# Kernel optimization log

Measured on AMD Instinct MI355X. Metric: run time of the kernel, lower is better.

The kernel has to match this reference:

```python
import jax, jax.numpy as jnp
import numpy as np

B, T, E = 4, 2048, 768
H = 12
D = E // H  # head dim = 64


def setup_inputs() -> dict:
    key = jax.random.key(0)
    ks = jax.random.split(key, 9)
    s = 0.02
    x = jax.random.normal(ks[0], (B, T, E), dtype=jnp.float32)
    Wq = jax.random.normal(ks[1], (E, E), dtype=jnp.float32) * s
    bq = jnp.zeros((E,), dtype=jnp.float32)
    Wk = jax.random.normal(ks[2], (E, E), dtype=jnp.float32) * s
    bk = jnp.zeros((E,), dtype=jnp.float32)
    Wv = jax.random.normal(ks[3], (E, E), dtype=jnp.float32) * s
    bv = jnp.zeros((E,), dtype=jnp.float32)
    Wo = jax.random.normal(ks[4], (E, E), dtype=jnp.float32) * s
    bo = jnp.zeros((E,), dtype=jnp.float32)
    # causal mask, broadcastable [1,1,T,T]; masked_fill where mask == 0
    attn_mask = jnp.tril(jnp.ones((T, T), dtype=jnp.int32))[None, None, :, :]
    return {"x": x, "Wq": Wq, "bq": bq, "Wk": Wk, "bk": bk,
            "Wv": Wv, "bv": bv, "Wo": Wo, "bo": bo, "attn_mask": attn_mask}


def reference(x, Wq, bq, Wk, bk, Wv, bv, Wo, bo, attn_mask):
    # QKV projections: [B,T,E] -> [B,T,E]
    q = x @ Wq + bq
    k = x @ Wk + bk
    v = x @ Wv + bv
    # split heads -> [B,H,T,D]
    def split(t):
        return t.reshape(B, T, H, D).transpose(0, 2, 1, 3)
    q, k, v = split(q), split(k), split(v)
    # eager attention: full [B,H,T,T] scores (faithful to the torch module)
    att = jnp.einsum('bhqd,bhkd->bhqk', q, k) * (1.0 / np.sqrt(D).astype(np.float32))
    att = jnp.where(attn_mask == 0, jnp.float32(-jnp.inf), att)
    att_weights = jax.nn.softmax(att, axis=-1)
    # attn_dropout rate = 0.0 (eval) -> identity
    y = jnp.einsum('bhqk,bhkd->bhqd', att_weights, v)
    y = y.transpose(0, 2, 1, 3).reshape(B, T, E)
    y = y @ Wo + bo  # proj_dropout rate = 0.0 -> identity
    return (y, att_weights)
```

## Files before the change

### kernel.cpp

```cpp
#include <hip/hip_runtime.h>
#include <hip/hip_bf16.h>
#include <stdint.h>

#define BB 4
#define HH 12
#define TT 2048
#define DD 64
#define EE 768
#define BT (BB*TT)
#define NQKV (3*EE)

typedef __attribute__((ext_vector_type(8))) short bf16x8;
typedef __attribute__((ext_vector_type(4))) float f32x4;

__device__ __forceinline__ unsigned short f2bf(float f){
  union { float f; unsigned int u; } x; x.f = f;
  unsigned int u = x.u;
  unsigned int r = (u + 0x7fffu + ((u >> 16) & 1u)) >> 16;
  return (unsigned short)r;
}

__global__ void cvt_bf16(const float* __restrict__ src, unsigned short* __restrict__ dst, int n){
  int i = (blockIdx.x*blockDim.x + threadIdx.x)*4;
  if (i < n){
    float4 v = *(const float4*)&src[i];
    ushort4 o;
    o.x = f2bf(v.x); o.y = f2bf(v.y); o.z = f2bf(v.z); o.w = f2bf(v.w);
    *(ushort4*)&dst[i] = o;
  }
}

__global__ void transpose_cvt_768(const float* __restrict__ src,
                                  unsigned short* __restrict__ dst){
  __shared__ float tile[32][33];
  int bx = blockIdx.x*32, by = blockIdx.y*32;
  int tx = threadIdx.x, ty = threadIdx.y;
  #pragma unroll
  for (int i=0;i<32;i+=8) tile[ty+i][tx] = src[(size_t)(by+ty+i)*EE + bx+tx];
  __syncthreads();
  #pragma unroll
  for (int i=0;i<32;i+=8) dst[(size_t)(bx+ty+i)*EE + by+tx] = f2bf(tile[tx][ty+i]);
}

__device__ __forceinline__ void gemm_core_128(
    const unsigned short* __restrict__ A, const unsigned short* __restrict__ Bt,
    int K, int mBase, int nBase,
    unsigned short* Alds, unsigned short* Blds,
    f32x4 acc[4][4])
{
  const int tid = threadIdx.x;
  const int lane = tid & 63, wave = tid >> 6;
  const int wm = wave & 1, wn = wave >> 1;
  const int ln15 = lane & 15, quad = lane >> 4;
  #pragma unroll
  for (int mt=0; mt<4; ++mt)
    #pragma unroll
    for (int nt=0; nt<4; ++nt)
      acc[mt][nt] = (f32x4){0.f,0.f,0.f,0.f};

  for (int k0=0; k0<K; k0+=32){
    #pragma unroll
    for (int i=0;i<2;i++){
      int idx = tid + i*256;
      int r = idx >> 2, seg = idx & 3;
      *(uint4*)&Alds[r*40 + seg*8] = *(const uint4*)&A[(size_t)(mBase + r)*K + k0 + seg*8];
      *(uint4*)&Blds[r*40 + seg*8] = *(const uint4*)&Bt[(size_t)(nBase + r)*K + k0 + seg*8];
    }
    __syncthreads();
    bf16x8 af[4], bfr[4];
    #pragma unroll
    for (int mt=0;mt<4;++mt) af[mt]  = *(const bf16x8*)&Alds[(wm*64 + mt*16 + ln15)*40 + quad*8];
    #pragma unroll
    for (int nt=0;nt<4;++nt) bfr[nt] = *(const bf16x8*)&Blds[(wn*64 + nt*16 + ln15)*40 + quad*8];
    #pragma unroll
    for (int mt=0;mt<4;++mt)
      #pragma unroll
      for (int nt=0;nt<4;++nt)
        acc[mt][nt] = __builtin_amdgcn_mfma_f32_16x16x32_bf16(af[mt], bfr[nt], acc[mt][nt], 0,0,0);
    __syncthreads();
  }
}

__global__ __launch_bounds__(256,2) void gemm_qkv(
    const unsigned short* __restrict__ x, const unsigned short* __restrict__ WtQKV,
    const float* __restrict__ bq, const float* __restrict__ bk,
    const float* __restrict__ bv,
    unsigned short* __restrict__ q_ws, unsigned short* __restrict__ k_ws,
    unsigned short* __restrict__ v_ws)
{
  __shared__ unsigned short Alds[128*40];
  __shared__ unsigned short Blds[128*40];
  const int mBase = blockIdx.y*128, nBase = blockIdx.x*128;
  f32x4 acc[4][4];
  gemm_core_128(x, WtQKV, EE, mBase, nBase, Alds, Blds, acc);

  const int tid = threadIdx.x, lane = tid&63, wave = tid>>6;
  const int wm = wave&1, wn = wave>>1, ln15 = lane&15, quad = lane>>4;
  const int which = nBase / EE;
  const float* bias = (which==0) ? bq : ((which==1) ? bk : bv);
  #pragma unroll
  for (int nt=0;nt<4;++nt){
    int col = nBase + wn*64 + nt*16 + ln15;
    int n0 = col - which*EE;
    int h = n0 >> 6, d = n0 & 63;
    float bsv = bias[n0];
    #pragma unroll
    for (int mt=0;mt<4;++mt){
      #pragma unroll
      for (int reg=0;reg<4;++reg){
        int row = mBase + wm*64 + mt*16 + quad*4 + reg;
        int b = row >> 11, t = row & 2047;
        unsigned short o = f2bf(acc[mt][nt][reg] + bsv);
        if (which==0)      q_ws[((size_t)(b*HH + h)*TT + t)*DD + d] = o;
        else if (which==1) k_ws[((size_t)(b*HH + h)*TT + t)*DD + d] = o;
        else               v_ws[((size_t)(b*HH + h)*DD + d)*TT + t] = o;
      }
    }
  }
}

__global__ __launch_bounds__(256,2) void gemm_proj(
    const unsigned short* __restrict__ yin, const unsigned short* __restrict__ WoT,
    const float* __restrict__ bo, float* __restrict__ out)
{
  __shared__ unsigned short Alds[128*40];
  __shared__ unsigned short Blds[128*40];
  const int mBase = blockIdx.y*128, nBase = blockIdx.x*128;
  f32x4 acc[4][4];
  gemm_core_128(yin, WoT, EE, mBase, nBase, Alds, Blds, acc);

  const int tid = threadIdx.x, lane = tid&63, wave = tid>>6;
  const int wm = wave&1, wn = wave>>1, ln15 = lane&15, quad = lane>>4;
  #pragma unroll
  for (int nt=0;nt<4;++nt){
    int col = nBase + wn*64 + nt*16 + ln15;
    float bsv = bo[col];
    #pragma unroll
    for (int mt=0;mt<4;++mt){
      #pragma unroll
      for (int reg=0;reg<4;++reg){
        int row = mBase + wm*64 + mt*16 + quad*4 + reg;
        out[(size_t)row*EE + col] = acc[mt][nt][reg] + bsv;
      }
    }
  }
}

__global__ __launch_bounds__(256,2) void attn_kernel(
    const unsigned short* __restrict__ q_ws, const unsigned short* __restrict__ k_ws,
    const unsigned short* __restrict__ v_ws, float* __restrict__ att,
    unsigned short* __restrict__ y_ws)
{
  const int qt = blockIdx.x;
  const int bh = blockIdx.y;
  const int b  = bh / HH, h = bh - b*HH;
  const int tid = threadIdx.x, lane = tid&63, wave = tid>>6;
  const int quad = lane>>4, ln15 = lane&15;

  __shared__ unsigned short Qs[64*72];
  __shared__ unsigned short Ks[64*72];
  __shared__ unsigned short Vts[64*72];
  __shared__ unsigned short Ps[4*16*72];

  const unsigned short* Qg = q_ws + ((size_t)bh*TT + qt*64)*DD;
  const unsigned short* Kg = k_ws + (size_t)bh*TT*DD;
  const unsigned short* Vg = v_ws + (size_t)bh*DD*TT;
  float* attb = att + ((size_t)bh*TT + (size_t)qt*64)*TT;

  #pragma unroll
  for (int i=0;i<2;i++){
    int idx = tid + i*256, r = idx>>3, seg = idx&7;
    *(uint4*)&Qs[r*72 + seg*8] = *(const uint4*)&Qg[(size_t)r*DD + seg*8];
  }
  __syncthreads();
  bf16x8 aq0 = *(const bf16x8*)&Qs[(wave*16+ln15)*72 + quad*8];
  bf16x8 aq1 = *(const bf16x8*)&Qs[(wave*16+ln15)*72 + 32 + quad*8];

  const float NEG = -30000.0f;
  const int qrow0 = qt*64 + wave*16 + quad*4;

  float l_i[4];
  #pragma unroll
  for (int r=0;r<4;++r) l_i[r] = 0.f;

  for (int kt=0; kt<=qt; ++kt){
    #pragma unroll
    for (int i=0;i<2;i++){
      int idx = tid + i*256, r = idx>>3, seg = idx&7;
      *(uint4*)&Ks[r*72 + seg*8] = *(const uint4*)&Kg[(size_t)(kt*64+r)*DD + seg*8];
    }
    __syncthreads();
    f32x4 s[4];
    #pragma unroll
    for (int nt=0;nt<4;++nt){
      s[nt] = (f32x4){0.f,0.f,0.f,0.f};
      bf16x8 bk0 = *(const bf16x8*)&Ks[(nt*16+ln15)*72 + quad*8];
      bf16x8 bk1 = *(const bf16x8*)&Ks[(nt*16+ln15)*72 + 32 + quad*8];
      s[nt] = __builtin_amdgcn_mfma_f32_16x16x32_bf16(aq0, bk0, s[nt], 0,0,0);
      s[nt] = __builtin_amdgcn_mfma_f32_16x16x32_bf16(aq1, bk1, s[nt], 0,0,0);
    }
    const bool diag = (kt==qt);
    #pragma unroll
    for (int reg=0;reg<4;++reg){
      float ss = 0.f;
      #pragma unroll
      for (int nt=0;nt<4;++nt){
        int key = kt*64 + nt*16 + ln15;
        float v = s[nt][reg]*0.125f;
        if (diag && key > qrow0+reg) v = NEG;
        ss += __expf(v);
      }
      ss += __shfl_xor(ss, 1);
      ss += __shfl_xor(ss, 2);
      ss += __shfl_xor(ss, 4);
      ss += __shfl_xor(ss, 8);
      l_i[reg] += ss;
    }
    __syncthreads();
  }
  float rl[4];
  #pragma unroll
  for (int r=0;r<4;++r) rl[r] = 1.f / l_i[r];

  f32x4 yacc[4];
  #pragma unroll
  for (int nt=0;nt<4;++nt) yacc[nt] = (f32x4){0.f,0.f,0.f,0.f};

  for (int kt=0; kt<=qt; ++kt){
    #pragma unroll
    for (int i=0;i<2;i++){
      int idx = tid + i*256, r = idx>>3, seg = idx&7;
      *(uint4*)&Ks[r*72 + seg*8]  = *(const uint4*)&Kg[(size_t)(kt*64+r)*DD + seg*8];
      *(uint4*)&Vts[r*72 + seg*8] = *(const uint4*)&Vg[(size_t)r*TT + kt*64 + seg*8];
    }
    __syncthreads();
    f32x4 s[4];
    #pragma unroll
    for (int nt=0;nt<4;++nt){
      s[nt] = (f32x4){0.f,0.f,0.f,0.f};
      bf16x8 bk0 = *(const bf16x8*)&Ks[(nt*16+ln15)*72 + quad*8];
      bf16x8 bk1 = *(const bf16x8*)&Ks[(nt*16+ln15)*72 + 32 + quad*8];
      s[nt] = __builtin_amdgcn_mfma_f32_16x16x32_bf16(aq0, bk0, s[nt], 0,0,0);
      s[nt] = __builtin_amdgcn_mfma_f32_16x16x32_bf16(aq1, bk1, s[nt], 0,0,0);
    }
    const bool diag = (kt==qt);
    #pragma unroll
    for (int nt=0;nt<4;++nt){
      int key = kt*64 + nt*16 + ln15;
      #pragma unroll
      for (int reg=0;reg<4;++reg){
        float v = s[nt][reg]*0.125f;
        if (diag && key > qrow0+reg) v = NEG;
        float p = __expf(v)*rl[reg];
        attb[(size_t)(wave*16 + quad*4 + reg)*TT + kt*64 + nt*16 + ln15] = p;
        Ps[wave*16*72 + (quad*4+reg)*72 + nt*16 + ln15] = f2bf(p);
      }
    }
    __syncthreads();
    bf16x8 ap0 = *(const bf16x8*)&Ps[(wave*16+ln15)*72 + quad*8];
    bf16x8 ap1 = *(const bf16x8*)&Ps[(wave*16+ln15)*72 + 32 + quad*8];
    #pragma unroll
    for (int nt=0;nt<4;++nt){
      bf16x8 bv0 = *(const bf16x8*)&Vts[(nt*16+ln15)*72 + quad*8];
      bf16x8 bv1 = *(const bf16x8*)&Vts[(nt*16+ln15)*72 + 32 + quad*8];
      yacc[nt] = __builtin_amdgcn_mfma_f32_16x16x32_bf16(ap0, bv0, yacc[nt], 0,0,0);
      yacc[nt] = __builtin_amdgcn_mfma_f32_16x16x32_bf16(ap1, bv1, yacc[nt], 0,0,0);
    }
    __syncthreads();
  }

  {
    int wstart = (qt+1)*64;
    int r = tid>>2;
    float4 z = make_float4(0.f,0.f,0.f,0.f);
    for (int c = wstart + (tid&3)*4; c < TT; c += 16)
      *(float4*)&attb[(size_t)r*TT + c] = z;
  }

  #pragma unroll
  for (int nt=0;nt<4;++nt){
    #pragma unroll
    for (int reg=0;reg<4;++reg){
      int t = qt*64 + wave*16 + quad*4 + reg;
      size_t row = (size_t)b*TT + t;
      int col = h*DD + nt*16 + ln15;
      y_ws[row*EE + col] = f2bf(yacc[nt][reg]);
    }
  }
}

extern "C" void kernel_launch(void* const* d_in, const int* in_sizes, int n_in,
                              void* d_out, int out_size, void* d_ws, size_t ws_size,
                              hipStream_t stream){
  (void)in_sizes; (void)n_in; (void)out_size; (void)ws_size;
  const float* x  = (const float*)d_in[0];
  const float* Wq = (const float*)d_in[1];
  const float* bq = (const float*)d_in[2];
  const float* Wk = (const float*)d_in[3];
  const float* bk = (const float*)d_in[4];
  const float* Wv = (const float*)d_in[5];
  const float* bv = (const float*)d_in[6];
  const float* Wo = (const float*)d_in[7];
  const float* bo = (const float*)d_in[8];

  float* out = (float*)d_out;
  float* y_out   = out;
  float* att_out = out + (size_t)BT*EE;

  unsigned short* ws = (unsigned short*)d_ws;
  unsigned short* x_bf   = ws;
  unsigned short* WtQKV  = x_bf  + (size_t)BT*EE;
  unsigned short* WoT    = WtQKV + (size_t)NQKV*EE;
  unsigned short* q_ws   = WoT   + (size_t)EE*EE;
  unsigned short* k_ws   = q_ws  + (size_t)BB*HH*TT*DD;
  unsigned short* v_ws   = k_ws  + (size_t)BB*HH*TT*DD;
  unsigned short* y_ws   = v_ws  + (size_t)BB*HH*TT*DD;

  cvt_bf16<<<(BT*EE)/(256*4), 256, 0, stream>>>(x, x_bf, BT*EE);
  dim3 tb(32,8), tg(24,24);
  transpose_cvt_768<<<tg, tb, 0, stream>>>(Wq, WtQKV);
  transpose_cvt_768<<<tg, tb, 0, stream>>>(Wk, WtQKV + (size_t)EE*EE);
  transpose_cvt_768<<<tg, tb, 0, stream>>>(Wv, WtQKV + (size_t)2*EE*EE);
  transpose_cvt_768<<<tg, tb, 0, stream>>>(Wo, WoT);

  gemm_qkv<<<dim3(NQKV/128, BT/128), 256, 0, stream>>>(x_bf, WtQKV, bq, bk, bv, q_ws, k_ws, v_ws);
  attn_kernel<<<dim3(TT/64, BB*HH), 256, 0, stream>>>(q_ws, k_ws, v_ws, att_out, y_ws);
  gemm_proj<<<dim3(EE/128, BT/128), 256, 0, stream>>>(y_ws, WoT, bo, y_out);
}
```

Measured before the change: 1.154 ms.

## Double-buffer K/V tiles, fold softmax scale into Q, remodel attention grid order

Folds the 1/sqrt(D)*log2(e) factor into Q in the QKV GEMM epilogue so attention can use exp2 with no per-element multiply. Double-buffers K and V in shared memory with register prefetch of the next tile, and drops one barrier per iteration. Defers the row-sum shuffle reduction to after the first pass. Remaps the 1D grid so groups of 8 heads share a query tile, meant to help cache locality for the K/V loads. Risks come from more shared memory use and the reduced synchronisation around the per-wave P buffer.

```diff
diff --git a/kernel.cpp b/kernel.cpp
--- a/kernel.cpp
+++ b/kernel.cpp
@@ -81,6 +81,7 @@
   }
 }
 
+#define QSCALE 0.18033688f
 __global__ __launch_bounds__(256,2) void gemm_qkv(
     const unsigned short* __restrict__ x, const unsigned short* __restrict__ WtQKV,
     const float* __restrict__ bq, const float* __restrict__ bk,
@@ -98,6 +99,7 @@
   const int wm = wave&1, wn = wave>>1, ln15 = lane&15, quad = lane>>4;
   const int which = nBase / EE;
   const float* bias = (which==0) ? bq : ((which==1) ? bk : bv);
+  const float sc = (which==0) ? QSCALE : 1.0f;
   #pragma unroll
   for (int nt=0;nt<4;++nt){
     int col = nBase + wn*64 + nt*16 + ln15;
@@ -110,7 +112,7 @@
       for (int reg=0;reg<4;++reg){
         int row = mBase + wm*64 + mt*16 + quad*4 + reg;
         int b = row >> 11, t = row & 2047;
-        unsigned short o = f2bf(acc[mt][nt][reg] + bsv);
+        unsigned short o = f2bf((acc[mt][nt][reg] + bsv)*sc);
         if (which==0)      q_ws[((size_t)(b*HH + h)*TT + t)*DD + d] = o;
         else if (which==1) k_ws[((size_t)(b*HH + h)*TT + t)*DD + d] = o;
         else               v_ws[((size_t)(b*HH + h)*DD + d)*TT + t] = o;
@@ -151,15 +153,16 @@
     const unsigned short* __restrict__ v_ws, float* __restrict__ att,
     unsigned short* __restrict__ y_ws)
 {
-  const int qt = blockIdx.x;
-  const int bh = blockIdx.y;
+  const int sid = blockIdx.x;
+  const int qt  = (sid >> 3) & 31;
+  const int bh  = (sid & 7) + ((sid >> 8) << 3);
   const int b  = bh / HH, h = bh - b*HH;
   const int tid = threadIdx.x, lane = tid&63, wave = tid>>6;
   const int quad = lane>>4, ln15 = lane&15;
 
   __shared__ unsigned short Qs[64*72];
-  __shared__ unsigned short Ks[64*72];
-  __shared__ unsigned short Vts[64*72];
+  __shared__ unsigned short Ks[2][64*72];
+  __shared__ unsigned short Vts[2][64*72];
   __shared__ unsigned short Ps[4*16*72];
 
   const unsigned short* Qg = q_ws + ((size_t)bh*TT + qt*64)*DD;
@@ -167,11 +170,14 @@
   const unsigned short* Vg = v_ws + (size_t)bh*DD*TT;
   float* attb = att + ((size_t)bh*TT + (size_t)qt*64)*TT;
 
-  #pragma unroll
-  for (int i=0;i<2;i++){
-    int idx = tid + i*256, r = idx>>3, seg = idx&7;
-    *(uint4*)&Qs[r*72 + seg*8] = *(const uint4*)&Qg[(size_t)r*DD + seg*8];
-  }
+  const int r0 = tid>>3, sg = tid&7;
+  const int r1 = r0 + 32;
+
+  uint4 ka0 = *(const uint4*)&Kg[(size_t)r0*DD + sg*8];
+  uint4 ka1 = *(const uint4*)&Kg[(size_t)r1*DD + sg*8];
+
+  *(uint4*)&Qs[r0*72 + sg*8] = *(const uint4*)&Qg[(size_t)r0*DD + sg*8];
+  *(uint4*)&Qs[r1*72 + sg*8] = *(const uint4*)&Qg[(size_t)r1*DD + sg*8];
   __syncthreads();
   bf16x8 aq0 = *(const bf16x8*)&Qs[(wave*16+ln15)*72 + quad*8];
   bf16x8 aq1 = *(const bf16x8*)&Qs[(wave*16+ln15)*72 + 32 + quad*8];
@@ -179,67 +185,77 @@
   const float NEG = -30000.0f;
   const int qrow0 = qt*64 + wave*16 + quad*4;
 
-  float l_i[4];
-  #pragma unroll
-  for (int r=0;r<4;++r) l_i[r] = 0.f;
-
+  float lp[4] = {0.f,0.f,0.f,0.f};
   for (int kt=0; kt<=qt; ++kt){
-    #pragma unroll
-    for (int i=0;i<2;i++){
-      int idx = tid + i*256, r = idx>>3, seg = idx&7;
-      *(uint4*)&Ks[r*72 + seg*8] = *(const uint4*)&Kg[(size_t)(kt*64+r)*DD + seg*8];
-    }
+    unsigned short* Kb = Ks[kt&1];
+    *(uint4*)&Kb[r0*72 + sg*8] = ka0;
+    *(uint4*)&Kb[r1*72 + sg*8] = ka1;
     __syncthreads();
+    if (kt < qt){
+      ka0 = *(const uint4*)&Kg[(size_t)((kt+1)*64+r0)*DD + sg*8];
+      ka1 = *(const uint4*)&Kg[(size_t)((kt+1)*64+r1)*DD + sg*8];
+    }
     f32x4 s[4];
     #pragma unroll
     for (int nt=0;nt<4;++nt){
       s[nt] = (f32x4){0.f,0.f,0.f,0.f};
-      bf16x8 bk0 = *(const bf16x8*)&Ks[(nt*16+ln15)*72 + quad*8];
-      bf16x8 bk1 = *(const bf16x8*)&Ks[(nt*16+ln15)*72 + 32 + quad*8];
+      bf16x8 bk0 = *(const bf16x8*)&Kb[(nt*16+ln15)*72 + quad*8];
+      bf16x8 bk1 = *(const bf16x8*)&Kb[(nt*16+ln15)*72 + 32 + quad*8];
       s[nt] = __builtin_amdgcn_mfma_f32_16x16x32_bf16(aq0, bk0, s[nt], 0,0,0);
       s[nt] = __builtin_amdgcn_mfma_f32_16x16x32_bf16(aq1, bk1, s[nt], 0,0,0);
     }
     const bool diag = (kt==qt);
     #pragma unroll
     for (int reg=0;reg<4;++reg){
-      float ss = 0.f;
       #pragma unroll
       for (int nt=0;nt<4;++nt){
-        int key = kt*64 + nt*16 + ln15;
-        float v = s[nt][reg]*0.125f;
-        if (diag && key > qrow0+reg) v = NEG;
-        ss += __expf(v);
+        float v = s[nt][reg];
+        if (diag && (kt*64 + nt*16 + ln15) > qrow0+reg) v = NEG;
+        lp[reg] += exp2f(v);
       }
-      ss += __shfl_xor(ss, 1);
-      ss += __shfl_xor(ss, 2);
-      ss += __shfl_xor(ss, 4);
-      ss += __shfl_xor(ss, 8);
-      l_i[reg] += ss;
-    }
+    }
+  }
+  float rl[4];
+  #pragma unroll
+  for (int r=0;r<4;++r){
+    float ss = lp[r];
+    ss += __shfl_xor(ss, 1);
+    ss += __shfl_xor(ss, 2);
+    ss += __shfl_xor(ss, 4);
+    ss += __shfl_xor(ss, 8);
+    rl[r] = 1.f / ss;
+  }
+
+  f32x4 yacc[4];
+  #pragma unroll
+  for (int nt=0;nt<4;++nt) yacc[nt] = (f32x4){0.f,0.f,0.f,0.f};
+
+  uint4 kb0 = *(const uint4*)&Kg[(size_t)r0*DD + sg*8];
+  uint4 kb1 = *(const uint4*)&Kg[(size_t)r1*DD + sg*8];
+  uint4 vb0 = *(const uint4*)&Vg[(size_t)r0*TT + sg*8];
+  uint4 vb1 = *(const uint4*)&Vg[(size_t)r1*TT + sg*8];
+  __syncthreads();
+
+  for (int kt=0; kt<=qt; ++kt){
+    unsigned short* Kb = Ks[kt&1];
+    unsigned short* Vb = Vts[kt&1];
+    *(uint4*)&Kb[r0*72 + sg*8] = kb0;
+    *(uint4*)&Kb[r1*72 + sg*8] = kb1;
+    *(uint4*)&Vb[r0*72 + sg*8] = vb0;
+    *(uint4*)&Vb[r1*72 + sg*8] = vb1;
     __syncthreads();
-  }
-  float rl[4];
-  #pragma unroll
-  for (int r=0;r<4;++r) rl[r] = 1.f / l_i[r];
-
-  f32x4 yacc[4];
-  #pragma unroll
-  for (int nt=0;nt<4;++nt) yacc[nt] = (f32x4){0.f,0.f,0.f,0.f};
-
-  for (int kt=0; kt<=qt; ++kt){
-    #pragma unroll
-    for (int i=0;i<2;i++){
-      int idx = tid + i*256, r = idx>>3, seg = idx&7;
-      *(uint4*)&Ks[r*72 + seg*8]  = *(const uint4*)&Kg[(size_t)(kt*64+r)*DD + seg*8];
-      *(uint4*)&Vts[r*72 + seg*8] = *(const uint4*)&Vg[(size_t)r*TT + kt*64 + seg*8];
-    }
-    __syncthreads();
+    if (kt < qt){
+      kb0 = *(const uint4*)&Kg[(size_t)((kt+1)*64+r0)*DD + sg*8];
+      kb1 = *(const uint4*)&Kg[(size_t)((kt+1)*64+r1)*DD + sg*8];
+      vb0 = *(const uint4*)&Vg[(size_t)r0*TT + (kt+1)*64 + sg*8];
+      vb1 = *(const uint4*)&Vg[(size_t)r1*TT + (kt+1)*64 + sg*8];
+    }
     f32x4 s[4];
     #pragma unroll
     for (int nt=0;nt<4;++nt){
       s[nt] = (f32x4){0.f,0.f,0.f,0.f};
-      bf16x8 bk0 = *(const bf16x8*)&Ks[(nt*16+ln15)*72 + quad*8];
-      bf16x8 bk1 = *(const bf16x8*)&Ks[(nt*16+ln15)*72 + 32 + quad*8];
+      bf16x8 bk0 = *(const bf16x8*)&Kb[(nt*16+ln15)*72 + quad*8];
+      bf16x8 bk1 = *(const bf16x8*)&Kb[(nt*16+ln15)*72 + 32 + quad*8];
       s[nt] = __builtin_amdgcn_mfma_f32_16x16x32_bf16(aq0, bk0, s[nt], 0,0,0);
       s[nt] = __builtin_amdgcn_mfma_f32_16x16x32_bf16(aq1, bk1, s[nt], 0,0,0);
     }
@@ -249,24 +265,22 @@
       int key = kt*64 + nt*16 + ln15;
       #pragma unroll
       for (int reg=0;reg<4;++reg){
-        float v = s[nt][reg]*0.125f;
+        float v = s[nt][reg];
         if (diag && key > qrow0+reg) v = NEG;
-        float p = __expf(v)*rl[reg];
-        attb[(size_t)(wave*16 + quad*4 + reg)*TT + kt*64 + nt*16 + ln15] = p;
-        Ps[wave*16*72 + (quad*4+reg)*72 + nt*16 + ln15] = f2bf(p);
+        float p = exp2f(v)*rl[reg];
+        attb[(size_t)(wave*16 + quad*4 + reg)*TT + key] = p;
+        Ps[wave*1152 + (quad*4+reg)*72 + nt*16 + ln15] = f2bf(p);
       }
     }
-    __syncthreads();
     bf16x8 ap0 = *(const bf16x8*)&Ps[(wave*16+ln15)*72 + quad*8];
     bf16x8 ap1 = *(const bf16x8*)&Ps[(wave*16+ln15)*72 + 32 + quad*8];
     #pragma unroll
     for (int nt=0;nt<4;++nt){
-      bf16x8 bv0 = *(const bf16x8*)&Vts[(nt*16+ln15)*72 + quad*8];
-      bf16x8 bv1 = *(const bf16x8*)&Vts[(nt*16+ln15)*72 + 32 + quad*8];
+      bf16x8 bv0 = *(const bf16x8*)&Vb[(nt*16+ln15)*72 + quad*8];
+      bf16x8 bv1 = *(const bf16x8*)&Vb[(nt*16+ln15)*72 + 32 + quad*8];
       yacc[nt] = __builtin_amdgcn_mfma_f32_16x16x32_bf16(ap0, bv0, yacc[nt], 0,0,0);
       yacc[nt] = __builtin_amdgcn_mfma_f32_16x16x32_bf16(ap1, bv1, yacc[nt], 0,0,0);
     }
-    __syncthreads();
   }
 
   {
@@ -324,6 +338,6 @@
   transpose_cvt_768<<<tg, tb, 0, stream>>>(Wo, WoT);
 
   gemm_qkv<<<dim3(NQKV/128, BT/128), 256, 0, stream>>>(x_bf, WtQKV, bq, bk, bv, q_ws, k_ws, v_ws);
-  attn_kernel<<<dim3(TT/64, BB*HH), 256, 0, stream>>>(q_ws, k_ws, v_ws, att_out, y_ws);
+  attn_kernel<<<dim3(32*BB*HH), 256, 0, stream>>>(q_ws, k_ws, v_ws, att_out, y_ws);
   gemm_proj<<<dim3(EE/128, BT/128), 256, 0, stream>>>(y_ws, WoT, bo, y_out);
 }
```

New measurement: 1.115 ms. 3.4% less time.
